# Performance work log

Measured on AMD Instinct MI355X. Metric: run time of the kernel, lower is better.

Reference implementation:

```python
import jax, jax.numpy as jnp
import numpy as np

EPS = 1e-8


def setup_inputs() -> dict:
    key = jax.random.key(0)
    k1, k2, k3, k4 = jax.random.split(key, 4)
    B, N, M, C = 512, 512, 128, 1024
    addr = M + 6  # read head: k(M) + beta(1) + g(1) + s(3) + gamma(1)
    controller_out = jax.random.normal(k1, (B, C), dtype=jnp.float32)
    prev_w = jax.random.uniform(k2, (B, N), dtype=jnp.float32)
    prev_w = prev_w / prev_w.sum(axis=1, keepdims=True)  # valid weighting
    memory_state = jax.random.normal(k3, (B, N, M), dtype=jnp.float32)
    W_fc = jax.random.normal(k4, (C, addr), dtype=jnp.float32) * 0.02
    b_fc = jnp.zeros((addr,), dtype=jnp.float32)
    return {"controller_out": controller_out, "prev_w": prev_w,
            "memory_state": memory_state, "W_fc": W_fc, "b_fc": b_fc}


def reference(controller_out, prev_w, memory_state, W_fc, b_fc):
    M = memory_state.shape[2]
    out = controller_out @ W_fc + b_fc  # [B, M+6]
    k = out[:, :M]                                   # key
    beta = jax.nn.softplus(out[:, M:M + 1])          # key strength
    g = jax.nn.sigmoid(out[:, M + 1:M + 2])          # interpolation gate
    s = jax.nn.softmax(out[:, M + 2:M + 5], axis=1)  # 3-tap shift weights
    gamma = 1.0 + jax.nn.softplus(out[:, M + 5:M + 6])

    # Content addressing (Eq. 5-6): cosine similarity + sharpened softmax
    norm_k = jnp.linalg.norm(k, axis=1, keepdims=True) + EPS      # [B,1]
    norm_mem = jnp.linalg.norm(memory_state, axis=2) + EPS        # [B,N]
    sim = jnp.einsum('bnm,bm->bn', memory_state, k) / (norm_k * norm_mem)
    w_c = jax.nn.softmax(beta * sim, axis=1)

    # Interpolation (Eq. 7)
    w_g = g * w_c + (1.0 - g) * prev_w

    # Circular 3-tap shift (Eq. 8): vectorized roll instead of per-slot loop
    w_s = (s[:, 0:1] * jnp.roll(w_g, 1, axis=1)
           + s[:, 1:2] * w_g
           + s[:, 2:3] * jnp.roll(w_g, -1, axis=1))

    # Sharpening (Eq. 9)
    w_pow = w_s ** gamma
    w = w_pow / (w_pow.sum(axis=1, keepdims=True) + EPS)

    # Read vector (read head)
    read_vec = jnp.einsum('bn,bnm->bm', w, memory_state)
    return (read_vec, w)
```

## Files before the change

### kernel.cpp

```cpp
#include <hip/hip_runtime.h>
#include <math.h>

#define BB   512
#define NN   512
#define MM   128
#define CC   1024
#define ADDR 134
#define EPSF 1e-8f
#define WSSTRIDE 136
#define EOFF  131072
#define POFF  (EOFF + BB * NN)

__device__ __forceinline__ float softplus_f(float x) {
    return fmaxf(x, 0.0f) + log1pf(expf(-fabsf(x)));
}

__global__ __launch_bounds__(192) void ntm_fc_kernel(
    const float* __restrict__ co,
    const float* __restrict__ W_fc,
    const float* __restrict__ b_fc,
    float* __restrict__ ws)
{
    __shared__ __align__(16) float s_co[2 * CC];
    __shared__ float s_nr[2][2];
    __shared__ float s_ex[2][8];

    const int t = threadIdx.x;
    const int b0 = blockIdx.x * 2;

    {
        const float4* src = (const float4*)(co + (size_t)b0 * CC);
        float4* dst = (float4*)s_co;
        for (int i = t; i < 512; i += 192) dst[i] = src[i];
    }
    __syncthreads();

    float k0 = 0.f, k1 = 0.f;
    if (t < ADDR) {
        float a00 = 0.f, a01 = 0.f, a10 = 0.f, a11 = 0.f;
        const float* Wj = W_fc + t;
        for (int c = 0; c < CC; c += 8) {
            float wv[8];
            #pragma unroll
            for (int i = 0; i < 8; ++i) wv[i] = Wj[(size_t)(c + i) * ADDR];
            #pragma unroll
            for (int i = 0; i < 8; ++i) {
                if (i & 1) { a01 = fmaf(wv[i], s_co[c + i], a01);
                             a11 = fmaf(wv[i], s_co[CC + c + i], a11); }
                else       { a00 = fmaf(wv[i], s_co[c + i], a00);
                             a10 = fmaf(wv[i], s_co[CC + c + i], a10); }
            }
        }
        float bias = b_fc[t];
        k0 = a00 + a01 + bias;
        k1 = a10 + a11 + bias;
        if (t >= MM) { s_ex[0][t - MM] = k0; s_ex[1][t - MM] = k1; }
        else {
            ws[(size_t)b0 * WSSTRIDE + t] = k0;
            ws[(size_t)(b0 + 1) * WSSTRIDE + t] = k1;
        }
    }
    if (t < MM) {
        float v0 = k0 * k0, v1 = k1 * k1;
        #pragma unroll
        for (int off = 32; off >= 1; off >>= 1) {
            v0 += __shfl_xor(v0, off, 64);
            v1 += __shfl_xor(v1, off, 64);
        }
        if ((t & 63) == 0) { s_nr[t >> 6][0] = v0; s_nr[t >> 6][1] = v1; }
    }
    __syncthreads();
    if (t < 2) {
        float ks = s_nr[0][t] + s_nr[1][t];
        float norm_k = sqrtf(ks) + EPSF;
        float beta = softplus_f(s_ex[t][0]);
        float g = 1.0f / (1.0f + expf(-s_ex[t][1]));
        float e0 = s_ex[t][2], e1 = s_ex[t][3], e2 = s_ex[t][4];
        float mx = fmaxf(e0, fmaxf(e1, e2));
        float x0 = expf(e0 - mx), x1 = expf(e1 - mx), x2 = expf(e2 - mx);
        float inv = 1.0f / (x0 + x1 + x2);
        float* p = ws + (size_t)(b0 + t) * WSSTRIDE + MM;
        p[0] = beta / norm_k;
        p[1] = g;
        p[2] = x0 * inv;
        p[3] = x1 * inv;
        p[4] = x2 * inv;
        p[5] = 1.0f + softplus_f(s_ex[t][5]);
    }
}

__global__ __launch_bounds__(256) void ntm_sim_kernel(
    const float* __restrict__ mem,
    float* __restrict__ ws)
{
    __shared__ __align__(16) float s_k[MM];
    __shared__ float s_red[4];
    __shared__ float s_bnk;

    const int t = threadIdx.x;
    const int bid = blockIdx.x;
    const int b = bid >> 2;
    const int rc = bid & 3;

    if (t < MM) s_k[t] = ws[(size_t)b * WSSTRIDE + t];
    if (t == MM) s_bnk = ws[(size_t)b * WSSTRIDE + MM];
    __syncthreads();

    const int l4 = t & 3;
    const int r  = t >> 2;
    float4 kf[8];
    #pragma unroll
    for (int i = 0; i < 8; ++i) kf[i] = ((const float4*)s_k)[l4 + 4 * i];
    const float bnk = s_bnk;
    const float4* memb = (const float4*)(mem + (size_t)b * NN * MM);

    float esum = 0.f;
    #pragma unroll
    for (int it = 0; it < 2; ++it) {
        const int row = rc * 128 + it * 64 + r;
        const float4* rp = memb + (size_t)row * 32;
        float4 a[8];
        #pragma unroll
        for (int i = 0; i < 8; ++i) a[i] = rp[l4 + 4 * i];
        float d = 0.f, q = 0.f;
        #pragma unroll
        for (int i = 0; i < 8; ++i) {
            d = fmaf(a[i].x, kf[i].x, d); q = fmaf(a[i].x, a[i].x, q);
            d = fmaf(a[i].y, kf[i].y, d); q = fmaf(a[i].y, a[i].y, q);
            d = fmaf(a[i].z, kf[i].z, d); q = fmaf(a[i].z, a[i].z, q);
            d = fmaf(a[i].w, kf[i].w, d); q = fmaf(a[i].w, a[i].w, q);
        }
        d += __shfl_xor(d, 1, 64); q += __shfl_xor(q, 1, 64);
        d += __shfl_xor(d, 2, 64); q += __shfl_xor(q, 2, 64);
        float e = expf(bnk * d / (sqrtf(q) + EPSF));
        if (l4 == 0) {
            ws[EOFF + (size_t)b * NN + row] = e;
            esum += e;
        }
    }
    #pragma unroll
    for (int off = 32; off >= 1; off >>= 1) esum += __shfl_xor(esum, off, 64);
    if ((t & 63) == 0) s_red[t >> 6] = esum;
    __syncthreads();
    if (t == 0)
        ws[POFF + bid] = s_red[0] + s_red[1] + s_red[2] + s_red[3];
}

__global__ __launch_bounds__(512) void ntm_read_kernel(
    const float* __restrict__ prev_w,
    const float* __restrict__ mem,
    const float* __restrict__ ws,
    float* __restrict__ out_rv,
    float* __restrict__ out_w)
{
    __shared__ float s_params[8];
    __shared__ float s_wg[NN];
    __shared__ float s_w[NN];
    __shared__ float s_red[8];
    __shared__ __align__(16) float s_part[16 * MM];

    const int t = threadIdx.x;
    const int b = blockIdx.x;

    float pw = prev_w[(size_t)b * NN + t];
    float e  = ws[EOFF + (size_t)b * NN + t];
    float S  = ws[POFF + b * 4 + 0] + ws[POFF + b * 4 + 1]
             + ws[POFF + b * 4 + 2] + ws[POFF + b * 4 + 3];
    if (t < 6) s_params[t] = ws[(size_t)b * WSSTRIDE + MM + t];
    __syncthreads();

    const float g = s_params[1];
    float wg = fmaf(g, e / S, (1.0f - g) * pw);
    s_wg[t] = wg;
    __syncthreads();

    float wsv = s_params[2] * s_wg[(t + NN - 1) & (NN - 1)]
              + s_params[3] * wg
              + s_params[4] * s_wg[(t + 1) & (NN - 1)];
    float wp = powf(wsv, s_params[5]);

    float lz = wp;
    #pragma unroll
    for (int off = 32; off >= 1; off >>= 1) lz += __shfl_xor(lz, off, 64);
    if ((t & 63) == 0) s_red[t >> 6] = lz;
    __syncthreads();
    float Z = 0.f;
    #pragma unroll
    for (int i = 0; i < 8; ++i) Z += s_red[i];

    float w = wp / (Z + EPSF);
    out_w[(size_t)b * NN + t] = w;
    s_w[t] = w;
    __syncthreads();

    {
        const int gp = t >> 5;
        const int l  = t & 31;
        const float4* memb = (const float4*)(mem + (size_t)b * NN * MM);
        float4 acc = make_float4(0.f, 0.f, 0.f, 0.f);
        for (int kk = 0; kk < 32; kk += 4) {
            const int r0 = gp + 16 * kk;
            float4 a0 = memb[(size_t)(r0      ) * 32 + l];
            float4 a1 = memb[(size_t)(r0 + 16 ) * 32 + l];
            float4 a2 = memb[(size_t)(r0 + 32 ) * 32 + l];
            float4 a3 = memb[(size_t)(r0 + 48 ) * 32 + l];
            float w0 = s_w[r0], w1 = s_w[r0 + 16], w2 = s_w[r0 + 32], w3 = s_w[r0 + 48];
            acc.x = fmaf(w0, a0.x, acc.x); acc.y = fmaf(w0, a0.y, acc.y);
            acc.z = fmaf(w0, a0.z, acc.z); acc.w = fmaf(w0, a0.w, acc.w);
            acc.x = fmaf(w1, a1.x, acc.x); acc.y = fmaf(w1, a1.y, acc.y);
            acc.z = fmaf(w1, a1.z, acc.z); acc.w = fmaf(w1, a1.w, acc.w);
            acc.x = fmaf(w2, a2.x, acc.x); acc.y = fmaf(w2, a2.y, acc.y);
            acc.z = fmaf(w2, a2.z, acc.z); acc.w = fmaf(w2, a2.w, acc.w);
            acc.x = fmaf(w3, a3.x, acc.x); acc.y = fmaf(w3, a3.y, acc.y);
            acc.z = fmaf(w3, a3.z, acc.z); acc.w = fmaf(w3, a3.w, acc.w);
        }
        *((float4*)&s_part[gp * MM + l * 4]) = acc;
        __syncthreads();
        if (t < MM) {
            float r = 0.f;
            #pragma unroll
            for (int q2 = 0; q2 < 16; ++q2) r += s_part[q2 * MM + t];
            out_rv[(size_t)b * MM + t] = r;
        }
    }
}

extern "C" void kernel_launch(void* const* d_in, const int* in_sizes, int n_in,
                              void* d_out, int out_size, void* d_ws, size_t ws_size,
                              hipStream_t stream) {
    const float* co     = (const float*)d_in[0];
    const float* prev_w = (const float*)d_in[1];
    const float* mem    = (const float*)d_in[2];
    const float* W_fc   = (const float*)d_in[3];
    const float* b_fc   = (const float*)d_in[4];
    float* out = (float*)d_out;
    float* ws  = (float*)d_ws;

    ntm_fc_kernel<<<BB / 2, 192, 0, stream>>>(co, W_fc, b_fc, ws);
    ntm_sim_kernel<<<BB * 4, 256, 0, stream>>>(mem, ws);
    ntm_read_kernel<<<BB, 512, 0, stream>>>(prev_w, mem, ws,
                                            out, out + (size_t)BB * MM);
}
```

Baseline: 264.6 us.

## Split read into slab-parallel kernel with atomics and use direct global-to-LDS loads

```diff
diff --git a/kernel.cpp b/kernel.cpp
--- a/kernel.cpp
+++ b/kernel.cpp
@@ -10,18 +10,26 @@
 #define WSSTRIDE 136
 #define EOFF  131072
 #define POFF  (EOFF + BB * NN)
+#define DOFF  (POFF + BB * 8)
 
 __device__ __forceinline__ float softplus_f(float x) {
     return fmaxf(x, 0.0f) + log1pf(expf(-fabsf(x)));
 }
 
-__global__ __launch_bounds__(192) void ntm_fc_kernel(
+__device__ __forceinline__ void gl2lds16(const float4* g, float4* l) {
+    __builtin_amdgcn_global_load_lds(
+        (const __attribute__((address_space(1))) void*)g,
+        (__attribute__((address_space(3))) void*)l, 16, 0, 0);
+}
+
+__global__ __launch_bounds__(384) void ntm_fc_kernel(
     const float* __restrict__ co,
     const float* __restrict__ W_fc,
     const float* __restrict__ b_fc,
     float* __restrict__ ws)
 {
     __shared__ __align__(16) float s_co[2 * CC];
+    __shared__ float s_fc[2][2][ADDR];
     __shared__ float s_nr[2][2];
     __shared__ float s_ex[2][8];
 
@@ -31,37 +39,48 @@
     {
         const float4* src = (const float4*)(co + (size_t)b0 * CC);
         float4* dst = (float4*)s_co;
-        for (int i = t; i < 512; i += 192) dst[i] = src[i];
-    }
-    __syncthreads();
-
-    float k0 = 0.f, k1 = 0.f;
+        for (int i = t; i < 512; i += 384) dst[i] = src[i];
+    }
+    __syncthreads();
+
+    {
+        const int grp = (t >= 192) ? 1 : 0;
+        const int j = t - grp * 192;
+        if (j < ADDR) {
+            float a00 = 0.f, a01 = 0.f, a10 = 0.f, a11 = 0.f;
+            const float* Wj = W_fc + j;
+            const int c0 = grp * 512;
+            for (int c = c0; c < c0 + 512; c += 8) {
+                float wv[8];
+                #pragma unroll
+                for (int i = 0; i < 8; ++i) wv[i] = Wj[(size_t)(c + i) * ADDR];
+                #pragma unroll
+                for (int i = 0; i < 8; ++i) {
+                    if (i & 1) { a01 = fmaf(wv[i], s_co[c + i], a01);
+                                 a11 = fmaf(wv[i], s_co[CC + c + i], a11); }
+                    else       { a00 = fmaf(wv[i], s_co[c + i], a00);
+                                 a10 = fmaf(wv[i], s_co[CC + c + i], a10); }
+                }
+            }
+            s_fc[grp][0][j] = a00 + a01;
+            s_fc[grp][1][j] = a10 + a11;
+        }
+    }
+    __syncthreads();
+
+    float r0 = 0.f, r1 = 0.f;
     if (t < ADDR) {
-        float a00 = 0.f, a01 = 0.f, a10 = 0.f, a11 = 0.f;
-        const float* Wj = W_fc + t;
-        for (int c = 0; c < CC; c += 8) {
-            float wv[8];
-            #pragma unroll
-            for (int i = 0; i < 8; ++i) wv[i] = Wj[(size_t)(c + i) * ADDR];
-            #pragma unroll
-            for (int i = 0; i < 8; ++i) {
-                if (i & 1) { a01 = fmaf(wv[i], s_co[c + i], a01);
-                             a11 = fmaf(wv[i], s_co[CC + c + i], a11); }
-                else       { a00 = fmaf(wv[i], s_co[c + i], a00);
-                             a10 = fmaf(wv[i], s_co[CC + c + i], a10); }
-            }
+        float bias = b_fc[t];
+        r0 = s_fc[0][0][t] + s_fc[1][0][t] + bias;
+        r1 = s_fc[0][1][t] + s_fc[1][1][t] + bias;
+        if (t >= MM) { s_ex[0][t - MM] = r0; s_ex[1][t - MM] = r1; }
+        else {
+            ws[(size_t)b0 * WSSTRIDE + t] = r0;
+            ws[(size_t)(b0 + 1) * WSSTRIDE + t] = r1;
         }
-        float bias = b_fc[t];
-        k0 = a00 + a01 + bias;
-        k1 = a10 + a11 + bias;
-        if (t >= MM) { s_ex[0][t - MM] = k0; s_ex[1][t - MM] = k1; }
-        else {
-            ws[(size_t)b0 * WSSTRIDE + t] = k0;
-            ws[(size_t)(b0 + 1) * WSSTRIDE + t] = k1;
-        }
     }
     if (t < MM) {
-        float v0 = k0 * k0, v1 = k1 * k1;
+        float v0 = r0 * r0, v1 = r1 * r1;
         #pragma unroll
         for (int off = 32; off >= 1; off >>= 1) {
             v0 += __shfl_xor(v0, off, 64);
@@ -89,83 +108,79 @@
     }
 }
 
-__global__ __launch_bounds__(256) void ntm_sim_kernel(
+__global__ __launch_bounds__(256, 2) void ntm_sim_kernel(
     const float* __restrict__ mem,
     float* __restrict__ ws)
 {
+    __shared__ __align__(16) float s_mem[64 * MM];
     __shared__ __align__(16) float s_k[MM];
     __shared__ float s_red[4];
     __shared__ float s_bnk;
 
     const int t = threadIdx.x;
     const int bid = blockIdx.x;
-    const int b = bid >> 2;
-    const int rc = bid & 3;
+    const int b = bid >> 3;
+    const int slab = bid & 7;
+
+    const float4* gslab = (const float4*)(mem + ((size_t)b * NN + slab * 64) * MM);
+    float4* l4p = (float4*)s_mem;
+    #pragma unroll
+    for (int i = 0; i < 8; ++i)
+        gl2lds16(gslab + i * 256 + t, l4p + i * 256 + t);
 
     if (t < MM) s_k[t] = ws[(size_t)b * WSSTRIDE + t];
     if (t == MM) s_bnk = ws[(size_t)b * WSSTRIDE + MM];
     __syncthreads();
 
     const int l4 = t & 3;
-    const int r  = t >> 2;
+    const int row = t >> 2;
+    const float4* k4 = (const float4*)s_k;
     float4 kf[8];
     #pragma unroll
-    for (int i = 0; i < 8; ++i) kf[i] = ((const float4*)s_k)[l4 + 4 * i];
-    const float bnk = s_bnk;
-    const float4* memb = (const float4*)(mem + (size_t)b * NN * MM);
-
-    float esum = 0.f;
-    #pragma unroll
-    for (int it = 0; it < 2; ++it) {
-        const int row = rc * 128 + it * 64 + r;
-        const float4* rp = memb + (size_t)row * 32;
-        float4 a[8];
-        #pragma unroll
-        for (int i = 0; i < 8; ++i) a[i] = rp[l4 + 4 * i];
-        float d = 0.f, q = 0.f;
-        #pragma unroll
-        for (int i = 0; i < 8; ++i) {
-            d = fmaf(a[i].x, kf[i].x, d); q = fmaf(a[i].x, a[i].x, q);
-            d = fmaf(a[i].y, kf[i].y, d); q = fmaf(a[i].y, a[i].y, q);
-            d = fmaf(a[i].z, kf[i].z, d); q = fmaf(a[i].z, a[i].z, q);
-            d = fmaf(a[i].w, kf[i].w, d); q = fmaf(a[i].w, a[i].w, q);
-        }
-        d += __shfl_xor(d, 1, 64); q += __shfl_xor(q, 1, 64);
-        d += __shfl_xor(d, 2, 64); q += __shfl_xor(q, 2, 64);
-        float e = expf(bnk * d / (sqrtf(q) + EPSF));
-        if (l4 == 0) {
-            ws[EOFF + (size_t)b * NN + row] = e;
-            esum += e;
-        }
-    }
-    #pragma unroll
-    for (int off = 32; off >= 1; off >>= 1) esum += __shfl_xor(esum, off, 64);
-    if ((t & 63) == 0) s_red[t >> 6] = esum;
-    __syncthreads();
-    if (t == 0)
-        ws[POFF + bid] = s_red[0] + s_red[1] + s_red[2] + s_red[3];
-}
-
-__global__ __launch_bounds__(512) void ntm_read_kernel(
+    for (int i = 0; i < 8; ++i) kf[i] = k4[l4 + 4 * i];
+
+    const float4* r4 = (const float4*)s_mem + (size_t)row * 32;
+    float d = 0.f, q = 0.f;
+    #pragma unroll
+    for (int i = 0; i < 8; ++i) {
+        float4 a = r4[l4 + 4 * i];
+        d = fmaf(a.x, kf[i].x, d); q = fmaf(a.x, a.x, q);
+        d = fmaf(a.y, kf[i].y, d); q = fmaf(a.y, a.y, q);
+        d = fmaf(a.z, kf[i].z, d); q = fmaf(a.z, a.z, q);
+        d = fmaf(a.w, kf[i].w, d); q = fmaf(a.w, a.w, q);
+    }
+    d += __shfl_xor(d, 1, 64); q += __shfl_xor(q, 1, 64);
+    d += __shfl_xor(d, 2, 64); q += __shfl_xor(q, 2, 64);
+
+    float e = expf(s_bnk * d / (sqrtf(q) + EPSF));
+    float el = (l4 == 0) ? e : 0.0f;
+    if (l4 == 0) ws[EOFF + (size_t)b * NN + slab * 64 + row] = e;
+
+    #pragma unroll
+    for (int off = 32; off >= 1; off >>= 1) el += __shfl_xor(el, off, 64);
+    if ((t & 63) == 0) s_red[t >> 6] = el;
+    __syncthreads();
+    if (t == 0) ws[POFF + bid] = s_red[0] + s_red[1] + s_red[2] + s_red[3];
+}
+
+__global__ __launch_bounds__(512) void ntm_w_kernel(
     const float* __restrict__ prev_w,
-    const float* __restrict__ mem,
-    const float* __restrict__ ws,
+    float* __restrict__ ws,
     float* __restrict__ out_rv,
     float* __restrict__ out_w)
 {
     __shared__ float s_params[8];
     __shared__ float s_wg[NN];
-    __shared__ float s_w[NN];
     __shared__ float s_red[8];
-    __shared__ __align__(16) float s_part[16 * MM];
 
     const int t = threadIdx.x;
     const int b = blockIdx.x;
 
     float pw = prev_w[(size_t)b * NN + t];
     float e  = ws[EOFF + (size_t)b * NN + t];
-    float S  = ws[POFF + b * 4 + 0] + ws[POFF + b * 4 + 1]
-             + ws[POFF + b * 4 + 2] + ws[POFF + b * 4 + 3];
+    float S = 0.f;
+    #pragma unroll
+    for (int i = 0; i < 8; ++i) S += ws[POFF + b * 8 + i];
     if (t < 6) s_params[t] = ws[(size_t)b * WSSTRIDE + MM + t];
     __syncthreads();
 
@@ -190,38 +205,54 @@
 
     float w = wp / (Z + EPSF);
     out_w[(size_t)b * NN + t] = w;
-    s_w[t] = w;
-    __syncthreads();
-
-    {
-        const int gp = t >> 5;
-        const int l  = t & 31;
-        const float4* memb = (const float4*)(mem + (size_t)b * NN * MM);
-        float4 acc = make_float4(0.f, 0.f, 0.f, 0.f);
-        for (int kk = 0; kk < 32; kk += 4) {
-            const int r0 = gp + 16 * kk;
-            float4 a0 = memb[(size_t)(r0      ) * 32 + l];
-            float4 a1 = memb[(size_t)(r0 + 16 ) * 32 + l];
-            float4 a2 = memb[(size_t)(r0 + 32 ) * 32 + l];
-            float4 a3 = memb[(size_t)(r0 + 48 ) * 32 + l];
-            float w0 = s_w[r0], w1 = s_w[r0 + 16], w2 = s_w[r0 + 32], w3 = s_w[r0 + 48];
-            acc.x = fmaf(w0, a0.x, acc.x); acc.y = fmaf(w0, a0.y, acc.y);
-            acc.z = fmaf(w0, a0.z, acc.z); acc.w = fmaf(w0, a0.w, acc.w);
-            acc.x = fmaf(w1, a1.x, acc.x); acc.y = fmaf(w1, a1.y, acc.y);
-            acc.z = fmaf(w1, a1.z, acc.z); acc.w = fmaf(w1, a1.w, acc.w);
-            acc.x = fmaf(w2, a2.x, acc.x); acc.y = fmaf(w2, a2.y, acc.y);
-            acc.z = fmaf(w2, a2.z, acc.z); acc.w = fmaf(w2, a2.w, acc.w);
-            acc.x = fmaf(w3, a3.x, acc.x); acc.y = fmaf(w3, a3.y, acc.y);
-            acc.z = fmaf(w3, a3.z, acc.z); acc.w = fmaf(w3, a3.w, acc.w);
-        }
-        *((float4*)&s_part[gp * MM + l * 4]) = acc;
-        __syncthreads();
-        if (t < MM) {
-            float r = 0.f;
-            #pragma unroll
-            for (int q2 = 0; q2 < 16; ++q2) r += s_part[q2 * MM + t];
-            out_rv[(size_t)b * MM + t] = r;
-        }
+    ws[DOFF + (size_t)b * NN + t] = w;
+    if (t < MM) out_rv[(size_t)b * MM + t] = 0.0f;
+}
+
+__global__ __launch_bounds__(256, 2) void ntm_read_kernel(
+    const float* __restrict__ mem,
+    const float* __restrict__ ws,
+    float* __restrict__ out_rv)
+{
+    __shared__ __align__(16) float s_mem[64 * MM];
+    __shared__ float s_w[64];
+    __shared__ __align__(16) float s_part[8 * MM];
+
+    const int t = threadIdx.x;
+    const int bid = blockIdx.x;
+    const int b = bid >> 3;
+    const int slab = bid & 7;
+
+    const float4* gslab = (const float4*)(mem + ((size_t)b * NN + slab * 64) * MM);
+    float4* l4p = (float4*)s_mem;
+    #pragma unroll
+    for (int i = 0; i < 8; ++i)
+        gl2lds16(gslab + i * 256 + t, l4p + i * 256 + t);
+
+    if (t < 64) s_w[t] = ws[DOFF + (size_t)b * NN + slab * 64 + t];
+    __syncthreads();
+
+    const int col4 = t & 31;
+    const int rg   = t >> 5;
+    const float4* m4 = (const float4*)s_mem;
+    float4 acc = make_float4(0.f, 0.f, 0.f, 0.f);
+    #pragma unroll
+    for (int m = 0; m < 8; ++m) {
+        const int r = rg * 8 + m;
+        float wv = s_w[r];
+        float4 a = m4[(size_t)r * 32 + col4];
+        acc.x = fmaf(wv, a.x, acc.x);
+        acc.y = fmaf(wv, a.y, acc.y);
+        acc.z = fmaf(wv, a.z, acc.z);
+        acc.w = fmaf(wv, a.w, acc.w);
+    }
+    ((float4*)s_part)[rg * 32 + col4] = acc;
+    __syncthreads();
+    if (t < MM) {
+        float v = 0.f;
+        #pragma unroll
+        for (int r = 0; r < 8; ++r) v += s_part[r * MM + t];
+        atomicAdd(&out_rv[(size_t)b * MM + t], v);
     }
 }
 
@@ -235,9 +266,11 @@
     const float* b_fc   = (const float*)d_in[4];
     float* out = (float*)d_out;
     float* ws  = (float*)d_ws;
-
-    ntm_fc_kernel<<<BB / 2, 192, 0, stream>>>(co, W_fc, b_fc, ws);
-    ntm_sim_kernel<<<BB * 4, 256, 0, stream>>>(mem, ws);
-    ntm_read_kernel<<<BB, 512, 0, stream>>>(prev_w, mem, ws,
-                                            out, out + (size_t)BB * MM);
-}
+    float* out_rv = out;
+    float* out_w  = out + (size_t)BB * MM;
+
+    ntm_fc_kernel<<<BB / 2, 384, 0, stream>>>(co, W_fc, b_fc, ws);
+    ntm_sim_kernel<<<BB * 8, 256, 0, stream>>>(mem, ws);
+    ntm_w_kernel<<<BB, 512, 0, stream>>>(prev_w, ws, out_rv, out_w);
+    ntm_read_kernel<<<BB * 8, 256, 0, stream>>>(mem, ws, out_rv);
+}
```

Result: faster. 255.9 us (-3.3%).
